# Kernel optimization log

Measured on AMD Instinct MI355X. Metric: run time of the kernel, lower is better.

## Reference

```python
import jax, jax.numpy as jnp
import numpy as np

E = 4
K = 2
BN_EPS = 1e-3


def _silu(y):
    return y * jax.nn.sigmoid(y)


def _bn_silu_nchw(y, g, b, m, v):
    # eval-mode BatchNorm2d over channel axis of [B, C, H, W], then SiLU
    scale = (g / jnp.sqrt(v + BN_EPS))[None, :, None, None]
    shift = (b - m * g / jnp.sqrt(v + BN_EPS))[None, :, None, None]
    return _silu(y * scale + shift)


def setup_inputs() -> dict:
    key = jax.random.key(0)
    ks = jax.random.split(key, 20)
    B, C1, C2, H, W = 32, 256, 256, 80, 80
    c_ = C2 // 2  # 128
    s = 0.05
    return {
        "x": jax.random.normal(ks[0], (B, C1, H, W), jnp.float32),
        "w1": jax.random.normal(ks[1], (c_, C1), jnp.float32) * s,
        "bn1_g": jax.random.uniform(ks[2], (c_,), jnp.float32, 0.5, 1.5),
        "bn1_b": jax.random.normal(ks[3], (c_,), jnp.float32) * s,
        "bn1_m": jax.random.normal(ks[4], (c_,), jnp.float32) * s,
        "bn1_v": jax.random.uniform(ks[5], (c_,), jnp.float32, 0.5, 1.5),
        "router_w": jax.random.normal(ks[6], (E, c_), jnp.float32) * s,
        "router_b": jax.random.normal(ks[7], (E,), jnp.float32) * s,
        "ew": jax.random.normal(ks[8], (E, c_, c_, 3, 3), jnp.float32) * s,
        "ebn_g": jax.random.uniform(ks[9], (E, c_), jnp.float32, 0.5, 1.5),
        "ebn_b": jax.random.normal(ks[10], (E, c_), jnp.float32) * s,
        "ebn_m": jax.random.normal(ks[11], (E, c_), jnp.float32) * s,
        "ebn_v": jax.random.uniform(ks[12], (E, c_), jnp.float32, 0.5, 1.5),
        "w3": jax.random.normal(ks[13], (C2, c_), jnp.float32) * s,
        "bn3_g": jax.random.uniform(ks[14], (C2,), jnp.float32, 0.5, 1.5),
        "bn3_b": jax.random.normal(ks[15], (C2,), jnp.float32) * s,
        "bn3_m": jax.random.normal(ks[16], (C2,), jnp.float32) * s,
        "bn3_v": jax.random.uniform(ks[17], (C2,), jnp.float32, 0.5, 1.5),
    }


def reference(x, w1, bn1_g, bn1_b, bn1_m, bn1_v, router_w, router_b,
              ew, ebn_g, ebn_b, ebn_m, ebn_v, w3, bn3_g, bn3_b, bn3_m, bn3_v):
    B, C1, H, W = x.shape
    c_ = w1.shape[0]

    # conv1: 1x1 conv + BN + SiLU -> [B, c_, H, W]
    x_in = _bn_silu_nchw(jnp.einsum('bchw,oc->bohw', x, w1), bn1_g, bn1_b, bn1_m, bn1_v)

    # flatten pixels to tokens [N, c_] (N = B*H*W), matching permute(0,2,3,1).reshape
    tokens = x_in.transpose(0, 2, 3, 1).reshape(-1, c_)
    N = tokens.shape[0]

    # router: 1x1 conv with bias -> per-token logits [N, E]
    logits = tokens @ router_w.T + router_b
    probs = jax.nn.softmax(logits, axis=-1)

    topw, topi = jax.lax.top_k(probs, K)                  # [N, K]
    topw = topw / jnp.sum(topw, axis=-1, keepdims=True)

    # dense [N, E] combine weights: normalized top-k weight where selected, else 0
    wd = jnp.zeros((N, E), tokens.dtype).at[jnp.arange(N)[:, None], topi].set(topw)

    # experts: 3x3 conv applied to 1x1 patches with pad=1 -> only center tap matters
    center = ew[:, :, :, 1, 1]                            # [E, c_out, c_in]
    ye = jnp.einsum('nc,eoc->neo', tokens, center)        # [N, E, c_]
    inv = ebn_g / jnp.sqrt(ebn_v + BN_EPS)                # [E, c_]
    ye = _silu(ye * inv[None] + (ebn_b - ebn_m * inv)[None])

    out_moe = jnp.einsum('neo,ne->no', ye, wd)            # weighted scatter-add
    out_moe = out_moe.reshape(B, H, W, c_).transpose(0, 3, 1, 2)

    # conv3: 1x1 conv + BN + SiLU -> [B, C2, H, W]
    x_out = _bn_silu_nchw(jnp.einsum('bchw,oc->bohw', out_moe, w3), bn3_g, bn3_b, bn3_m, bn3_v)

    # shortcut (c1 == c2 here)
    return x_out + x
```

## Files before the change

kernel.cpp:

```cpp
#include <hip/hip_runtime.h>
#include <cstdint>
#include <cstddef>

#define NEXP 4
#define CH   128
#define C1   256
#define C2   256
#define HWSZ 6400
#define NTOKS 204800
#define BNE  1e-3f

using f32x4 = __attribute__((ext_vector_type(4))) float;
using f16x8 = __attribute__((ext_vector_type(8))) _Float16;
using s16x8 = __attribute__((ext_vector_type(8))) short;

static __device__ __forceinline__ unsigned short f2bf(float f) {
    union { float f; unsigned u; } v; v.f = f;
    unsigned r = v.u + 0x7fffu + ((v.u >> 16) & 1u);
    return (unsigned short)(r >> 16);
}
static __device__ __forceinline__ f32x4 zero4() {
    f32x4 z; z[0] = 0.f; z[1] = 0.f; z[2] = 0.f; z[3] = 0.f; return z;
}

__global__ __launch_bounds__(256) void k0_pack_center(const float* __restrict__ ew,
                                                      unsigned short* __restrict__ cen) {
    int idx = blockIdx.x * 256 + threadIdx.x;
    if (idx < NEXP * CH * CH) cen[idx] = f2bf(ew[(size_t)idx * 9 + 4]);
}

__global__ __launch_bounds__(256, 2) void k1_conv1_router(
    const float* __restrict__ x, const float* __restrict__ w1,
    const float* __restrict__ bn1_g, const float* __restrict__ bn1_b,
    const float* __restrict__ bn1_m, const float* __restrict__ bn1_v,
    const float* __restrict__ rw, const float* __restrict__ rb,
    unsigned short* __restrict__ tokens, float* __restrict__ wd)
{
    const int tid  = threadIdx.x;
    const int lane = tid & 63;
    const int wv   = tid >> 6;
    const int n15  = lane & 15;
    const int quad = lane >> 4;

    const int nt0 = blockIdx.x * 64;
    const int b   = nt0 / HWSZ;
    const int hw0 = nt0 % HWSZ;

    __shared__ union {
        struct { _Float16 Ah[128 * 40]; _Float16 Al[128 * 40];
                 _Float16 Bh[64 * 40];  _Float16 Bl[64 * 40]; } s;
        struct { float tok[64 * 129]; float logit[64 * 4]; } e;
    } u;
    __shared__ float s1_l[128], t1_l[128];

    if (tid < 128) {
        float s = bn1_g[tid] / sqrtf(bn1_v[tid] + BNE);
        s1_l[tid] = s;
        t1_l[tid] = bn1_b[tid] - bn1_m[tid] * s;
    }

    f32x4 acc_m[2][4], acc_c[2][4];
    #pragma unroll
    for (int i = 0; i < 2; i++)
        #pragma unroll
        for (int j = 0; j < 4; j++) { acc_m[i][j] = zero4(); acc_c[i][j] = zero4(); }

    for (int kc = 0; kc < C1; kc += 32) {
        #pragma unroll
        for (int rep = 0; rep < 4; rep++) {
            int lin = rep * 256 + tid;
            int o   = lin >> 3;
            int k4  = (lin & 7) * 4;
            const float4 v = *(const float4*)&w1[(size_t)o * C1 + kc + k4];
            _Float16* ah = &u.s.Ah[o * 40 + k4];
            _Float16* al = &u.s.Al[o * 40 + k4];
            _Float16 h0 = (_Float16)v.x, h1 = (_Float16)v.y, h2 = (_Float16)v.z, h3 = (_Float16)v.w;
            ah[0] = h0; ah[1] = h1; ah[2] = h2; ah[3] = h3;
            al[0] = (_Float16)((v.x - (float)h0) * 2048.0f);
            al[1] = (_Float16)((v.y - (float)h1) * 2048.0f);
            al[2] = (_Float16)((v.z - (float)h2) * 2048.0f);
            al[3] = (_Float16)((v.w - (float)h3) * 2048.0f);
        }
        {
            int i  = tid & 63;
            int kg = tid >> 6;
            #pragma unroll
            for (int r = 0; r < 2; r++) {
                int k4 = (kg * 2 + r) * 4;
                const float* xp = x + ((size_t)(b * C1 + kc + k4)) * HWSZ + hw0 + i;
                float v0 = xp[0], v1 = xp[HWSZ], v2 = xp[2 * HWSZ], v3 = xp[3 * HWSZ];
                _Float16* bh = &u.s.Bh[i * 40 + k4];
                _Float16* bl = &u.s.Bl[i * 40 + k4];
                _Float16 h0 = (_Float16)v0, h1 = (_Float16)v1, h2 = (_Float16)v2, h3 = (_Float16)v3;
                bh[0] = h0; bh[1] = h1; bh[2] = h2; bh[3] = h3;
                bl[0] = (_Float16)((v0 - (float)h0) * 2048.0f);
                bl[1] = (_Float16)((v1 - (float)h1) * 2048.0f);
                bl[2] = (_Float16)((v2 - (float)h2) * 2048.0f);
                bl[3] = (_Float16)((v3 - (float)h3) * 2048.0f);
            }
        }
        __syncthreads();

        f16x8 a_h[2], a_l[2], b_h[4], b_l[4];
        #pragma unroll
        for (int mt = 0; mt < 2; mt++) {
            int row = (wv * 2 + mt) * 16 + n15;
            a_h[mt] = *(const f16x8*)&u.s.Ah[row * 40 + quad * 8];
            a_l[mt] = *(const f16x8*)&u.s.Al[row * 40 + quad * 8];
        }
        #pragma unroll
        for (int nt = 0; nt < 4; nt++) {
            int row = nt * 16 + n15;
            b_h[nt] = *(const f16x8*)&u.s.Bh[row * 40 + quad * 8];
            b_l[nt] = *(const f16x8*)&u.s.Bl[row * 40 + quad * 8];
        }
        #pragma unroll
        for (int mt = 0; mt < 2; mt++)
            #pragma unroll
            for (int nt = 0; nt < 4; nt++) {
                acc_m[mt][nt] = __builtin_amdgcn_mfma_f32_16x16x32_f16(a_h[mt], b_h[nt], acc_m[mt][nt], 0, 0, 0);
                acc_c[mt][nt] = __builtin_amdgcn_mfma_f32_16x16x32_f16(a_l[mt], b_h[nt], acc_c[mt][nt], 0, 0, 0);
                acc_c[mt][nt] = __builtin_amdgcn_mfma_f32_16x16x32_f16(a_h[mt], b_l[nt], acc_c[mt][nt], 0, 0, 0);
            }
        __syncthreads();
    }

    #pragma unroll
    for (int mt = 0; mt < 2; mt++)
        #pragma unroll
        for (int nt = 0; nt < 4; nt++)
            #pragma unroll
            for (int r = 0; r < 4; r++) {
                int o  = (wv * 2 + mt) * 16 + quad * 4 + r;
                int tk = nt * 16 + n15;
                float y1 = acc_m[mt][nt][r] + acc_c[mt][nt][r] * (1.0f / 2048.0f);
                float y  = y1 * s1_l[o] + t1_l[o];
                u.e.tok[tk * 129 + o] = y / (1.0f + expf(-y));
            }
    __syncthreads();

    {
        int tk = tid >> 2;
        int e  = tid & 3;
        const float* trow = &u.e.tok[tk * 129];
        const float* wrow = &rw[e * CH];
        float a0 = 0.f, a1 = 0.f, a2 = 0.f, a3 = 0.f;
        #pragma unroll 8
        for (int c = 0; c < CH; c += 4) {
            a0 = fmaf(trow[c + 0], wrow[c + 0], a0);
            a1 = fmaf(trow[c + 1], wrow[c + 1], a1);
            a2 = fmaf(trow[c + 2], wrow[c + 2], a2);
            a3 = fmaf(trow[c + 3], wrow[c + 3], a3);
        }
        u.e.logit[tk * 4 + e] = ((a0 + a1) + (a2 + a3)) + rb[e];
    }
    __syncthreads();

    if (tid < 64) {
        const float* lg = &u.e.logit[tid * 4];
        float l0 = lg[0], l1 = lg[1], l2 = lg[2], l3 = lg[3];
        int i1 = 0; float m1 = l0;
        if (l1 > m1) { m1 = l1; i1 = 1; }
        if (l2 > m1) { m1 = l2; i1 = 2; }
        if (l3 > m1) { m1 = l3; i1 = 3; }
        int i2 = -1; float m2 = -3.4e38f;
        if (i1 != 0 && l0 > m2) { m2 = l0; i2 = 0; }
        if (i1 != 1 && l1 > m2) { m2 = l1; i2 = 1; }
        if (i1 != 2 && l2 > m2) { m2 = l2; i2 = 2; }
        if (i1 != 3 && l3 > m2) { m2 = l3; i2 = 3; }
        float p2 = expf(m2 - m1);
        float wa = 1.0f / (1.0f + p2);
        float wb = p2 * wa;
        float4 wout;
        wout.x = (i1 == 0) ? wa : ((i2 == 0) ? wb : 0.0f);
        wout.y = (i1 == 1) ? wa : ((i2 == 1) ? wb : 0.0f);
        wout.z = (i1 == 2) ? wa : ((i2 == 2) ? wb : 0.0f);
        wout.w = (i1 == 3) ? wa : ((i2 == 3) ? wb : 0.0f);
        *(float4*)&wd[(size_t)(nt0 + tid) * 4] = wout;
    }

    #pragma unroll
    for (int rep = 0; rep < 8; rep++) {
        int lin = rep * 256 + tid;
        int n   = lin >> 5;
        int c4  = (lin & 31) * 4;
        const float* tp = &u.e.tok[n * 129 + c4];
        ushort4 pk;
        pk.x = f2bf(tp[0]); pk.y = f2bf(tp[1]); pk.z = f2bf(tp[2]); pk.w = f2bf(tp[3]);
        *(ushort4*)&tokens[(size_t)(nt0 + n) * CH + c4] = pk;
    }
}

__global__ __launch_bounds__(256, 2) void k2_experts(
    const unsigned short* __restrict__ tokens, const unsigned short* __restrict__ cen,
    const float* __restrict__ wd,
    const float* __restrict__ ebn_g, const float* __restrict__ ebn_b,
    const float* __restrict__ ebn_m, const float* __restrict__ ebn_v,
    unsigned short* __restrict__ moe)
{
    const int tid  = threadIdx.x;
    const int lane = tid & 63;
    const int wv   = tid >> 6;
    const int n15  = lane & 15;
    const int quad = lane >> 4;
    const int nt0  = blockIdx.x * 64;

    __shared__ unsigned short Bt[64 * 136];
    __shared__ unsigned short Ac[128 * 136];
    __shared__ float wd_l[256];
    __shared__ float inv_l[512], sh_l[512];

    #pragma unroll
    for (int rep = 0; rep < 4; rep++) {
        int lin = rep * 256 + tid;
        int n   = lin >> 4;
        int c8  = (lin & 15) * 8;
        *(uint4*)&Bt[n * 136 + c8] = *(const uint4*)&tokens[(size_t)(nt0 + n) * CH + c8];
    }
    wd_l[tid] = wd[(size_t)nt0 * 4 + tid];
    #pragma unroll
    for (int r = 0; r < 2; r++) {
        int idx = r * 256 + tid;
        float iv = ebn_g[idx] / sqrtf(ebn_v[idx] + BNE);
        inv_l[idx] = iv;
        sh_l[idx]  = ebn_b[idx] - ebn_m[idx] * iv;
    }

    f32x4 oacc[2][4];
    #pragma unroll
    for (int i = 0; i < 2; i++)
        #pragma unroll
        for (int j = 0; j < 4; j++) oacc[i][j] = zero4();

    for (int e = 0; e < NEXP; e++) {
        __syncthreads();
        #pragma unroll
        for (int rep = 0; rep < 8; rep++) {
            int lin = rep * 256 + tid;
            int o   = lin >> 4;
            int c8  = (lin & 15) * 8;
            *(uint4*)&Ac[o * 136 + c8] = *(const uint4*)&cen[(size_t)e * CH * CH + o * CH + c8];
        }
        __syncthreads();

        f32x4 acc[2][4];
        #pragma unroll
        for (int i = 0; i < 2; i++)
            #pragma unroll
            for (int j = 0; j < 4; j++) acc[i][j] = zero4();

        #pragma unroll
        for (int kk = 0; kk < 4; kk++) {
            int ko = kk * 32 + quad * 8;
            s16x8 a0 = *(const s16x8*)&Ac[((wv * 2 + 0) * 16 + n15) * 136 + ko];
            s16x8 a1 = *(const s16x8*)&Ac[((wv * 2 + 1) * 16 + n15) * 136 + ko];
            s16x8 b0 = *(const s16x8*)&Bt[(0 * 16 + n15) * 136 + ko];
            s16x8 b1 = *(const s16x8*)&Bt[(1 * 16 + n15) * 136 + ko];
            s16x8 b2 = *(const s16x8*)&Bt[(2 * 16 + n15) * 136 + ko];
            s16x8 b3 = *(const s16x8*)&Bt[(3 * 16 + n15) * 136 + ko];
            acc[0][0] = __builtin_amdgcn_mfma_f32_16x16x32_bf16(a0, b0, acc[0][0], 0, 0, 0);
            acc[0][1] = __builtin_amdgcn_mfma_f32_16x16x32_bf16(a0, b1, acc[0][1], 0, 0, 0);
            acc[0][2] = __builtin_amdgcn_mfma_f32_16x16x32_bf16(a0, b2, acc[0][2], 0, 0, 0);
            acc[0][3] = __builtin_amdgcn_mfma_f32_16x16x32_bf16(a0, b3, acc[0][3], 0, 0, 0);
            acc[1][0] = __builtin_amdgcn_mfma_f32_16x16x32_bf16(a1, b0, acc[1][0], 0, 0, 0);
            acc[1][1] = __builtin_amdgcn_mfma_f32_16x16x32_bf16(a1, b1, acc[1][1], 0, 0, 0);
            acc[1][2] = __builtin_amdgcn_mfma_f32_16x16x32_bf16(a1, b2, acc[1][2], 0, 0, 0);
            acc[1][3] = __builtin_amdgcn_mfma_f32_16x16x32_bf16(a1, b3, acc[1][3], 0, 0, 0);
        }

        #pragma unroll
        for (int mt = 0; mt < 2; mt++)
            #pragma unroll
            for (int nt = 0; nt < 4; nt++) {
                float wde = wd_l[(nt * 16 + n15) * 4 + e];
                #pragma unroll
                for (int r = 0; r < 4; r++) {
                    int o = (wv * 2 + mt) * 16 + quad * 4 + r;
                    float y = acc[mt][nt][r] * inv_l[e * CH + o] + sh_l[e * CH + o];
                    oacc[mt][nt][r] += wde * (y / (1.0f + __expf(-y)));
                }
            }
    }

    #pragma unroll
    for (int mt = 0; mt < 2; mt++)
        #pragma unroll
        for (int nt = 0; nt < 4; nt++) {
            int tk = nt * 16 + n15;
            int ob = (wv * 2 + mt) * 16 + quad * 4;
            ushort4 pk;
            pk.x = f2bf(oacc[mt][nt][0]); pk.y = f2bf(oacc[mt][nt][1]);
            pk.z = f2bf(oacc[mt][nt][2]); pk.w = f2bf(oacc[mt][nt][3]);
            *(ushort4*)&moe[(size_t)(nt0 + tk) * CH + ob] = pk;
        }
}

__global__ __launch_bounds__(256, 2) void k3_conv3(
    const unsigned short* __restrict__ moe, const float* __restrict__ w3,
    const float* __restrict__ bn3_g, const float* __restrict__ bn3_b,
    const float* __restrict__ bn3_m, const float* __restrict__ bn3_v,
    const float* __restrict__ x, float* __restrict__ out)
{
    const int tid  = threadIdx.x;
    const int lane = tid & 63;
    const int wv   = tid >> 6;
    const int n15  = lane & 15;
    const int quad = lane >> 4;
    const int nt0  = blockIdx.x * 64;
    const int b    = nt0 / HWSZ;
    const int hw0  = nt0 % HWSZ;

    __shared__ unsigned short A3[256 * 40];
    __shared__ unsigned short B3[64 * 40];
    __shared__ float s3_l[256], t3_l[256];

    {
        float s = bn3_g[tid] / sqrtf(bn3_v[tid] + BNE);
        s3_l[tid] = s;
        t3_l[tid] = bn3_b[tid] - bn3_m[tid] * s;
    }

    f32x4 acc[4][4];
    #pragma unroll
    for (int i = 0; i < 4; i++)
        #pragma unroll
        for (int j = 0; j < 4; j++) acc[i][j] = zero4();

    for (int kc = 0; kc < CH; kc += 32) {
        #pragma unroll
        for (int rep = 0; rep < 8; rep++) {
            int lin = rep * 256 + tid;
            int o   = lin >> 3;
            int k4  = (lin & 7) * 4;
            const float4 v = *(const float4*)&w3[(size_t)o * CH + kc + k4];
            ushort4 pk;
            pk.x = f2bf(v.x); pk.y = f2bf(v.y); pk.z = f2bf(v.z); pk.w = f2bf(v.w);
            *(ushort4*)&A3[o * 40 + k4] = pk;
        }
        #pragma unroll
        for (int rep = 0; rep < 2; rep++) {
            int lin = rep * 256 + tid;
            int n   = lin >> 3;
            int k4  = (lin & 7) * 4;
            *(ushort4*)&B3[n * 40 + k4] = *(const ushort4*)&moe[(size_t)(nt0 + n) * CH + kc + k4];
        }
        __syncthreads();

        s16x8 bf[4];
        #pragma unroll
        for (int nt = 0; nt < 4; nt++)
            bf[nt] = *(const s16x8*)&B3[(nt * 16 + n15) * 40 + quad * 8];
        #pragma unroll
        for (int mt = 0; mt < 4; mt++) {
            s16x8 af = *(const s16x8*)&A3[((wv * 4 + mt) * 16 + n15) * 40 + quad * 8];
            #pragma unroll
            for (int nt = 0; nt < 4; nt++)
                acc[mt][nt] = __builtin_amdgcn_mfma_f32_16x16x32_bf16(af, bf[nt], acc[mt][nt], 0, 0, 0);
        }
        __syncthreads();
    }

    #pragma unroll
    for (int mt = 0; mt < 4; mt++)
        #pragma unroll
        for (int nt = 0; nt < 4; nt++)
            #pragma unroll
            for (int r = 0; r < 4; r++) {
                int o2 = (wv * 4 + mt) * 16 + quad * 4 + r;
                int tk = nt * 16 + n15;
                size_t g = ((size_t)(b * C2 + o2)) * HWSZ + hw0 + tk;
                float y = acc[mt][nt][r] * s3_l[o2] + t3_l[o2];
                out[g] = y / (1.0f + __expf(-y)) + x[g];
            }
}

extern "C" void kernel_launch(void* const* d_in, const int* in_sizes, int n_in,
                              void* d_out, int out_size, void* d_ws, size_t ws_size,
                              hipStream_t stream) {
    const float* x     = (const float*)d_in[0];
    const float* w1    = (const float*)d_in[1];
    const float* bn1_g = (const float*)d_in[2];
    const float* bn1_b = (const float*)d_in[3];
    const float* bn1_m = (const float*)d_in[4];
    const float* bn1_v = (const float*)d_in[5];
    const float* rw    = (const float*)d_in[6];
    const float* rb    = (const float*)d_in[7];
    const float* ew    = (const float*)d_in[8];
    const float* ebn_g = (const float*)d_in[9];
    const float* ebn_b = (const float*)d_in[10];
    const float* ebn_m = (const float*)d_in[11];
    const float* ebn_v = (const float*)d_in[12];
    const float* w3    = (const float*)d_in[13];
    const float* bn3_g = (const float*)d_in[14];
    const float* bn3_b = (const float*)d_in[15];
    const float* bn3_m = (const float*)d_in[16];
    const float* bn3_v = (const float*)d_in[17];
    float* out = (float*)d_out;

    char* ws = (char*)d_ws;
    unsigned short* tokens = (unsigned short*)(ws);
    unsigned short* moe    = (unsigned short*)(ws + 52428800);
    float*          wdv    = (float*)(ws + 104857600);
    unsigned short* cen    = (unsigned short*)(ws + 104857600 + 3276800);

    k0_pack_center<<<dim3(256),  dim3(256), 0, stream>>>(ew, cen);
    k1_conv1_router<<<dim3(3200), dim3(256), 0, stream>>>(x, w1, bn1_g, bn1_b, bn1_m, bn1_v,
                                                          rw, rb, tokens, wdv);
    k2_experts<<<dim3(3200), dim3(256), 0, stream>>>(tokens, cen, wdv,
                                                     ebn_g, ebn_b, ebn_m, ebn_v, moe);
    k3_conv3<<<dim3(3200), dim3(256), 0, stream>>>(moe, w3, bn3_g, bn3_b, bn3_m, bn3_v, x, out);
    (void)in_sizes; (void)n_in; (void)out_size; (void)ws_size;
}
```

Measured before the change: 680.9 us.

## Pre-pack conv weights once, load via global_load_lds, double expert token tile

Weight conversion for conv1 (hi/lo fp16 split) and conv3 (bf16) moves into a single prepack kernel that writes them in a chunked, unpadded layout. The GEMM kernels then stream each weight chunk straight into LDS with global_load_lds instead of having every block convert fp32 weights. The expert kernel now processes 128 tokens per block with a 2x2 wave split, which doubles reuse of the expert weight tile and halves the number of blocks. The tradeoff is more LDS and registers in the expert kernel, and unpadded LDS rows that may cause bank conflicts.

```diff
diff --git a/kernel.cpp b/kernel.cpp
--- a/kernel.cpp
+++ b/kernel.cpp
@@ -22,15 +22,41 @@
 static __device__ __forceinline__ f32x4 zero4() {
     f32x4 z; z[0] = 0.f; z[1] = 0.f; z[2] = 0.f; z[3] = 0.f; return z;
 }
-
-__global__ __launch_bounds__(256) void k0_pack_center(const float* __restrict__ ew,
-                                                      unsigned short* __restrict__ cen) {
-    int idx = blockIdx.x * 256 + threadIdx.x;
-    if (idx < NEXP * CH * CH) cen[idx] = f2bf(ew[(size_t)idx * 9 + 4]);
+static __device__ __forceinline__ void g2lds16(const void* g, void* l) {
+    __builtin_amdgcn_global_load_lds(
+        (const __attribute__((address_space(1))) void*)g,
+        (__attribute__((address_space(3))) void*)l, 16, 0, 0);
+}
+
+__global__ __launch_bounds__(256) void k0_pack(const float* __restrict__ ew,
+                                               const float* __restrict__ w1,
+                                               const float* __restrict__ w3,
+                                               unsigned short* __restrict__ cen,
+                                               _Float16* __restrict__ w1s,
+                                               unsigned short* __restrict__ w3p) {
+    int bid = blockIdx.x;
+    int tid = threadIdx.x;
+    if (bid < 256) {
+        int idx = bid * 256 + tid;
+        cen[idx] = f2bf(ew[(size_t)idx * 9 + 4]);
+    } else if (bid < 384) {
+        int lin = (bid - 256) * 256 + tid;
+        int o = lin >> 8, k = lin & 255;
+        int s = k >> 5, kk = k & 31;
+        float v = w1[o * C1 + k];
+        _Float16 h = (_Float16)v;
+        w1s[((s * 2 + 0) * 128 + o) * 32 + kk] = h;
+        w1s[((s * 2 + 1) * 128 + o) * 32 + kk] = (_Float16)((v - (float)h) * 2048.0f);
+    } else {
+        int lin = (bid - 384) * 256 + tid;
+        int o = lin >> 7, k = lin & 127;
+        int s = k >> 5, kk = k & 31;
+        w3p[(s * 256 + o) * 32 + kk] = f2bf(w3[o * CH + k]);
+    }
 }
 
 __global__ __launch_bounds__(256, 2) void k1_conv1_router(
-    const float* __restrict__ x, const float* __restrict__ w1,
+    const float* __restrict__ x, const _Float16* __restrict__ w1s,
     const float* __restrict__ bn1_g, const float* __restrict__ bn1_b,
     const float* __restrict__ bn1_m, const float* __restrict__ bn1_v,
     const float* __restrict__ rw, const float* __restrict__ rb,
@@ -38,17 +64,17 @@
 {
     const int tid  = threadIdx.x;
     const int lane = tid & 63;
-    const int wv   = tid >> 6;
     const int n15  = lane & 15;
     const int quad = lane >> 4;
+    const int wv   = tid >> 6;
 
     const int nt0 = blockIdx.x * 64;
     const int b   = nt0 / HWSZ;
     const int hw0 = nt0 % HWSZ;
 
     __shared__ union {
-        struct { _Float16 Ah[128 * 40]; _Float16 Al[128 * 40];
-                 _Float16 Bh[64 * 40];  _Float16 Bl[64 * 40]; } s;
+        struct { _Float16 Ahl[2 * 128 * 32];
+                 _Float16 Bh[64 * 40]; _Float16 Bl[64 * 40]; } s;
         struct { float tok[64 * 129]; float logit[64 * 4]; } e;
     } u;
     __shared__ float s1_l[128], t1_l[128];
@@ -65,21 +91,17 @@
         #pragma unroll
         for (int j = 0; j < 4; j++) { acc_m[i][j] = zero4(); acc_c[i][j] = zero4(); }
 
-    for (int kc = 0; kc < C1; kc += 32) {
-        #pragma unroll
-        for (int rep = 0; rep < 4; rep++) {
-            int lin = rep * 256 + tid;
-            int o   = lin >> 3;
-            int k4  = (lin & 7) * 4;
-            const float4 v = *(const float4*)&w1[(size_t)o * C1 + kc + k4];
-            _Float16* ah = &u.s.Ah[o * 40 + k4];
-            _Float16* al = &u.s.Al[o * 40 + k4];
-            _Float16 h0 = (_Float16)v.x, h1 = (_Float16)v.y, h2 = (_Float16)v.z, h3 = (_Float16)v.w;
-            ah[0] = h0; ah[1] = h1; ah[2] = h2; ah[3] = h3;
-            al[0] = (_Float16)((v.x - (float)h0) * 2048.0f);
-            al[1] = (_Float16)((v.y - (float)h1) * 2048.0f);
-            al[2] = (_Float16)((v.z - (float)h2) * 2048.0f);
-            al[3] = (_Float16)((v.w - (float)h3) * 2048.0f);
+    const char* w1b = (const char*)w1s;
+    char*       Ab  = (char*)u.s.Ahl;
+
+    for (int s = 0; s < 8; s++) {
+        {
+            const char* src = w1b + s * 16384 + tid * 16;
+            char*       dst = Ab + tid * 16;
+            g2lds16(src + 0,     dst + 0);
+            g2lds16(src + 4096,  dst + 4096);
+            g2lds16(src + 8192,  dst + 8192);
+            g2lds16(src + 12288, dst + 12288);
         }
         {
             int i  = tid & 63;
@@ -87,7 +109,7 @@
             #pragma unroll
             for (int r = 0; r < 2; r++) {
                 int k4 = (kg * 2 + r) * 4;
-                const float* xp = x + ((size_t)(b * C1 + kc + k4)) * HWSZ + hw0 + i;
+                const float* xp = x + ((size_t)(b * C1 + s * 32 + k4)) * HWSZ + hw0 + i;
                 float v0 = xp[0], v1 = xp[HWSZ], v2 = xp[2 * HWSZ], v3 = xp[3 * HWSZ];
                 _Float16* bh = &u.s.Bh[i * 40 + k4];
                 _Float16* bl = &u.s.Bl[i * 40 + k4];
@@ -101,27 +123,25 @@
         }
         __syncthreads();
 
-        f16x8 a_h[2], a_l[2], b_h[4], b_l[4];
+        f16x8 a_h[2], a_l[2];
         #pragma unroll
         for (int mt = 0; mt < 2; mt++) {
             int row = (wv * 2 + mt) * 16 + n15;
-            a_h[mt] = *(const f16x8*)&u.s.Ah[row * 40 + quad * 8];
-            a_l[mt] = *(const f16x8*)&u.s.Al[row * 40 + quad * 8];
+            a_h[mt] = *(const f16x8*)&u.s.Ahl[row * 32 + quad * 8];
+            a_l[mt] = *(const f16x8*)&u.s.Ahl[4096 + row * 32 + quad * 8];
         }
         #pragma unroll
         for (int nt = 0; nt < 4; nt++) {
             int row = nt * 16 + n15;
-            b_h[nt] = *(const f16x8*)&u.s.Bh[row * 40 + quad * 8];
-            b_l[nt] = *(const f16x8*)&u.s.Bl[row * 40 + quad * 8];
-        }
-        #pragma unroll
-        for (int mt = 0; mt < 2; mt++)
-            #pragma unroll
-            for (int nt = 0; nt < 4; nt++) {
-                acc_m[mt][nt] = __builtin_amdgcn_mfma_f32_16x16x32_f16(a_h[mt], b_h[nt], acc_m[mt][nt], 0, 0, 0);
-                acc_c[mt][nt] = __builtin_amdgcn_mfma_f32_16x16x32_f16(a_l[mt], b_h[nt], acc_c[mt][nt], 0, 0, 0);
-                acc_c[mt][nt] = __builtin_amdgcn_mfma_f32_16x16x32_f16(a_h[mt], b_l[nt], acc_c[mt][nt], 0, 0, 0);
-            }
+            f16x8 b_h = *(const f16x8*)&u.s.Bh[row * 40 + quad * 8];
+            f16x8 b_l = *(const f16x8*)&u.s.Bl[row * 40 + quad * 8];
+            #pragma unroll
+            for (int mt = 0; mt < 2; mt++) {
+                acc_m[mt][nt] = __builtin_amdgcn_mfma_f32_16x16x32_f16(a_h[mt], b_h, acc_m[mt][nt], 0, 0, 0);
+                acc_c[mt][nt] = __builtin_amdgcn_mfma_f32_16x16x32_f16(a_l[mt], b_h, acc_c[mt][nt], 0, 0, 0);
+                acc_c[mt][nt] = __builtin_amdgcn_mfma_f32_16x16x32_f16(a_h[mt], b_l, acc_c[mt][nt], 0, 0, 0);
+            }
+        }
         __syncthreads();
     }
 
@@ -203,21 +223,24 @@
     const int wv   = tid >> 6;
     const int n15  = lane & 15;
     const int quad = lane >> 4;
-    const int nt0  = blockIdx.x * 64;
-
-    __shared__ unsigned short Bt[64 * 136];
+    const int qm   = wv & 1;
+    const int qn   = wv >> 1;
+    const int nt0  = blockIdx.x * 128;
+
+    __shared__ unsigned short Bt[128 * 136];
     __shared__ unsigned short Ac[128 * 136];
-    __shared__ float wd_l[256];
+    __shared__ float wd_l[512];
     __shared__ float inv_l[512], sh_l[512];
 
     #pragma unroll
-    for (int rep = 0; rep < 4; rep++) {
+    for (int rep = 0; rep < 8; rep++) {
         int lin = rep * 256 + tid;
         int n   = lin >> 4;
         int c8  = (lin & 15) * 8;
         *(uint4*)&Bt[n * 136 + c8] = *(const uint4*)&tokens[(size_t)(nt0 + n) * CH + c8];
     }
-    wd_l[tid] = wd[(size_t)nt0 * 4 + tid];
+    wd_l[tid]       = wd[(size_t)nt0 * 4 + tid];
+    wd_l[256 + tid] = wd[(size_t)nt0 * 4 + 256 + tid];
     #pragma unroll
     for (int r = 0; r < 2; r++) {
         int idx = r * 256 + tid;
@@ -226,9 +249,9 @@
         sh_l[idx]  = ebn_b[idx] - ebn_m[idx] * iv;
     }
 
-    f32x4 oacc[2][4];
-    #pragma unroll
-    for (int i = 0; i < 2; i++)
+    f32x4 oacc[4][4];
+    #pragma unroll
+    for (int i = 0; i < 4; i++)
         #pragma unroll
         for (int j = 0; j < 4; j++) oacc[i][j] = zero4();
 
@@ -243,39 +266,36 @@
         }
         __syncthreads();
 
-        f32x4 acc[2][4];
-        #pragma unroll
-        for (int i = 0; i < 2; i++)
+        f32x4 acc[4][4];
+        #pragma unroll
+        for (int i = 0; i < 4; i++)
             #pragma unroll
             for (int j = 0; j < 4; j++) acc[i][j] = zero4();
 
         #pragma unroll
         for (int kk = 0; kk < 4; kk++) {
             int ko = kk * 32 + quad * 8;
-            s16x8 a0 = *(const s16x8*)&Ac[((wv * 2 + 0) * 16 + n15) * 136 + ko];
-            s16x8 a1 = *(const s16x8*)&Ac[((wv * 2 + 1) * 16 + n15) * 136 + ko];
-            s16x8 b0 = *(const s16x8*)&Bt[(0 * 16 + n15) * 136 + ko];
-            s16x8 b1 = *(const s16x8*)&Bt[(1 * 16 + n15) * 136 + ko];
-            s16x8 b2 = *(const s16x8*)&Bt[(2 * 16 + n15) * 136 + ko];
-            s16x8 b3 = *(const s16x8*)&Bt[(3 * 16 + n15) * 136 + ko];
-            acc[0][0] = __builtin_amdgcn_mfma_f32_16x16x32_bf16(a0, b0, acc[0][0], 0, 0, 0);
-            acc[0][1] = __builtin_amdgcn_mfma_f32_16x16x32_bf16(a0, b1, acc[0][1], 0, 0, 0);
-            acc[0][2] = __builtin_amdgcn_mfma_f32_16x16x32_bf16(a0, b2, acc[0][2], 0, 0, 0);
-            acc[0][3] = __builtin_amdgcn_mfma_f32_16x16x32_bf16(a0, b3, acc[0][3], 0, 0, 0);
-            acc[1][0] = __builtin_amdgcn_mfma_f32_16x16x32_bf16(a1, b0, acc[1][0], 0, 0, 0);
-            acc[1][1] = __builtin_amdgcn_mfma_f32_16x16x32_bf16(a1, b1, acc[1][1], 0, 0, 0);
-            acc[1][2] = __builtin_amdgcn_mfma_f32_16x16x32_bf16(a1, b2, acc[1][2], 0, 0, 0);
-            acc[1][3] = __builtin_amdgcn_mfma_f32_16x16x32_bf16(a1, b3, acc[1][3], 0, 0, 0);
-        }
-
-        #pragma unroll
-        for (int mt = 0; mt < 2; mt++)
+            s16x8 a[4], bb[4];
+            #pragma unroll
+            for (int i = 0; i < 4; i++) {
+                a[i]  = *(const s16x8*)&Ac[(qm * 64 + i * 16 + n15) * 136 + ko];
+                bb[i] = *(const s16x8*)&Bt[(qn * 64 + i * 16 + n15) * 136 + ko];
+            }
+            #pragma unroll
+            for (int mt = 0; mt < 4; mt++)
+                #pragma unroll
+                for (int nt = 0; nt < 4; nt++)
+                    acc[mt][nt] = __builtin_amdgcn_mfma_f32_16x16x32_bf16(a[mt], bb[nt], acc[mt][nt], 0, 0, 0);
+        }
+
+        #pragma unroll
+        for (int mt = 0; mt < 4; mt++)
             #pragma unroll
             for (int nt = 0; nt < 4; nt++) {
-                float wde = wd_l[(nt * 16 + n15) * 4 + e];
+                float wde = wd_l[(qn * 64 + nt * 16 + n15) * 4 + e];
                 #pragma unroll
                 for (int r = 0; r < 4; r++) {
-                    int o = (wv * 2 + mt) * 16 + quad * 4 + r;
+                    int o = qm * 64 + mt * 16 + quad * 4 + r;
                     float y = acc[mt][nt][r] * inv_l[e * CH + o] + sh_l[e * CH + o];
                     oacc[mt][nt][r] += wde * (y / (1.0f + __expf(-y)));
                 }
@@ -283,11 +303,11 @@
     }
 
     #pragma unroll
-    for (int mt = 0; mt < 2; mt++)
+    for (int mt = 0; mt < 4; mt++)
         #pragma unroll
         for (int nt = 0; nt < 4; nt++) {
-            int tk = nt * 16 + n15;
-            int ob = (wv * 2 + mt) * 16 + quad * 4;
+            int tk = qn * 64 + nt * 16 + n15;
+            int ob = qm * 64 + mt * 16 + quad * 4;
             ushort4 pk;
             pk.x = f2bf(oacc[mt][nt][0]); pk.y = f2bf(oacc[mt][nt][1]);
             pk.z = f2bf(oacc[mt][nt][2]); pk.w = f2bf(oacc[mt][nt][3]);
@@ -296,7 +316,7 @@
 }
 
 __global__ __launch_bounds__(256, 2) void k3_conv3(
-    const unsigned short* __restrict__ moe, const float* __restrict__ w3,
+    const unsigned short* __restrict__ moe, const unsigned short* __restrict__ w3p,
     const float* __restrict__ bn3_g, const float* __restrict__ bn3_b,
     const float* __restrict__ bn3_m, const float* __restrict__ bn3_v,
     const float* __restrict__ x, float* __restrict__ out)
@@ -310,7 +330,7 @@
     const int b    = nt0 / HWSZ;
     const int hw0  = nt0 % HWSZ;
 
-    __shared__ unsigned short A3[256 * 40];
+    __shared__ unsigned short A3[256 * 32];
     __shared__ unsigned short B3[64 * 40];
     __shared__ float s3_l[256], t3_l[256];
 
@@ -326,23 +346,24 @@
         #pragma unroll
         for (int j = 0; j < 4; j++) acc[i][j] = zero4();
 
-    for (int kc = 0; kc < CH; kc += 32) {
-        #pragma unroll
-        for (int rep = 0; rep < 8; rep++) {
-            int lin = rep * 256 + tid;
-            int o   = lin >> 3;
-            int k4  = (lin & 7) * 4;
-            const float4 v = *(const float4*)&w3[(size_t)o * CH + kc + k4];
-            ushort4 pk;
-            pk.x = f2bf(v.x); pk.y = f2bf(v.y); pk.z = f2bf(v.z); pk.w = f2bf(v.w);
-            *(ushort4*)&A3[o * 40 + k4] = pk;
+    const char* w3b = (const char*)w3p;
+    char*       Ab  = (char*)A3;
+
+    for (int s = 0; s < 4; s++) {
+        {
+            const char* src = w3b + s * 16384 + tid * 16;
+            char*       dst = Ab + tid * 16;
+            g2lds16(src + 0,     dst + 0);
+            g2lds16(src + 4096,  dst + 4096);
+            g2lds16(src + 8192,  dst + 8192);
+            g2lds16(src + 12288, dst + 12288);
         }
         #pragma unroll
         for (int rep = 0; rep < 2; rep++) {
             int lin = rep * 256 + tid;
             int n   = lin >> 3;
             int k4  = (lin & 7) * 4;
-            *(ushort4*)&B3[n * 40 + k4] = *(const ushort4*)&moe[(size_t)(nt0 + n) * CH + kc + k4];
+            *(ushort4*)&B3[n * 40 + k4] = *(const ushort4*)&moe[(size_t)(nt0 + n) * CH + s * 32 + k4];
         }
         __syncthreads();
 
@@ -352,7 +373,7 @@
             bf[nt] = *(const s16x8*)&B3[(nt * 16 + n15) * 40 + quad * 8];
         #pragma unroll
         for (int mt = 0; mt < 4; mt++) {
-            s16x8 af = *(const s16x8*)&A3[((wv * 4 + mt) * 16 + n15) * 40 + quad * 8];
+            s16x8 af = *(const s16x8*)&A3[((wv * 4 + mt) * 16 + n15) * 32 + quad * 8];
             #pragma unroll
             for (int nt = 0; nt < 4; nt++)
                 acc[mt][nt] = __builtin_amdgcn_mfma_f32_16x16x32_bf16(af, bf[nt], acc[mt][nt], 0, 0, 0);
@@ -401,13 +422,15 @@
     unsigned short* tokens = (unsigned short*)(ws);
     unsigned short* moe    = (unsigned short*)(ws + 52428800);
     float*          wdv    = (float*)(ws + 104857600);
-    unsigned short* cen    = (unsigned short*)(ws + 104857600 + 3276800);
-
-    k0_pack_center<<<dim3(256),  dim3(256), 0, stream>>>(ew, cen);
-    k1_conv1_router<<<dim3(3200), dim3(256), 0, stream>>>(x, w1, bn1_g, bn1_b, bn1_m, bn1_v,
+    unsigned short* cen    = (unsigned short*)(ws + 108134400);
+    _Float16*       w1s    = (_Float16*)(ws + 108265472);
+    unsigned short* w3p    = (unsigned short*)(ws + 108396544);
+
+    k0_pack<<<dim3(512), dim3(256), 0, stream>>>(ew, w1, w3, cen, w1s, w3p);
+    k1_conv1_router<<<dim3(3200), dim3(256), 0, stream>>>(x, w1s, bn1_g, bn1_b, bn1_m, bn1_v,
                                                           rw, rb, tokens, wdv);
-    k2_experts<<<dim3(3200), dim3(256), 0, stream>>>(tokens, cen, wdv,
+    k2_experts<<<dim3(1600), dim3(256), 0, stream>>>(tokens, cen, wdv,
                                                      ebn_g, ebn_b, ebn_m, ebn_v, moe);
-    k3_conv3<<<dim3(3200), dim3(256), 0, stream>>>(moe, w3, bn3_g, bn3_b, bn3_m, bn3_v, x, out);
+    k3_conv3<<<dim3(3200), dim3(256), 0, stream>>>(moe, w3p, bn3_g, bn3_b, bn3_m, bn3_v, x, out);
     (void)in_sizes; (void)n_in; (void)out_size; (void)ws_size;
 }
```

Result: faster. 643.0 us (-5.6%).
